# Performance work log

Measured on AMD Instinct MI355X. Metric: run time of the kernel, lower is better.

The kernel has to match this reference:

```python
import jax, jax.numpy as jnp
import numpy as np

B, S, P, D, H, R = 2, 2048, 1024, 2048, 16, 16
DH = D // H  # 128


def _rope(t, cos, sin):
    # t: [B,S,H,DH]; cos/sin: [S, DH//2]; complex pair rotation
    t2 = t.reshape(t.shape[0], t.shape[1], t.shape[2], DH // 2, 2)
    a, b = t2[..., 0], t2[..., 1]
    c = cos[None, :, None, :]
    s = sin[None, :, None, :]
    out = jnp.stack([a * c - b * s, a * s + b * c], axis=-1)
    return out.reshape(t.shape)


def setup_inputs() -> dict:
    key = jax.random.key(0)
    ks = jax.random.split(key, 16)
    sc = 1.0 / np.sqrt(D)
    inv_freq = 1.0 / (10000.0 ** (np.arange(0, DH, 2, dtype=np.float32) / DH))
    pos = (P + np.arange(S, dtype=np.float32))[:, None] * inv_freq[None, :]
    i_idx = np.arange(S)[:, None]
    j_idx = np.arange(P + S)[None, :]
    mask = np.where(j_idx <= P + i_idx, 0.0, -1e9).astype(np.float32)
    return {
        "x": jax.random.normal(ks[0], (B, S, D), jnp.float32),
        "freqs_cos": jnp.asarray(np.cos(pos)),
        "freqs_sin": jnp.asarray(np.sin(pos)),
        "mask": jnp.asarray(mask)[None, None],
        "prev_key": jax.random.normal(ks[1], (B, P, H, DH), jnp.float32),
        "prev_value": jax.random.normal(ks[2], (B, P, H, DH), jnp.float32),
        "pooled_scale": jax.random.uniform(ks[3], (B, 1), jnp.float32),
        "wq": jax.random.normal(ks[4], (D, D), jnp.float32) * sc,
        "wk": jax.random.normal(ks[5], (D, D), jnp.float32) * sc,
        "wv": jax.random.normal(ks[6], (D, D), jnp.float32) * sc,
        "wo": jax.random.normal(ks[7], (D, D), jnp.float32) * sc,
        "wq_A": jax.random.normal(ks[8], (D, R), jnp.float32) * sc,
        "wq_B": jax.random.normal(ks[9], (R, D), jnp.float32) * 0.02,
        "wk_A": jax.random.normal(ks[10], (D, R), jnp.float32) * sc,
        "wk_B": jax.random.normal(ks[11], (R, D), jnp.float32) * 0.02,
        "wv_A": jax.random.normal(ks[12], (D, R), jnp.float32) * sc,
        "wv_B": jax.random.normal(ks[13], (R, D), jnp.float32) * 0.02,
        "wo_A": jax.random.normal(ks[14], (D, R), jnp.float32) * sc,
        "wo_B": jax.random.normal(ks[15], (R, D), jnp.float32) * 0.02,
    }


def reference(x, freqs_cos, freqs_sin, mask, prev_key, prev_value, pooled_scale,
              wq, wk, wv, wo, wq_A, wq_B, wk_A, wk_B, wv_A, wv_B, wo_A, wo_B):
    ps = pooled_scale[:, None, :]  # [B,1,1] per-batch LoRA scale
    xq = x @ wq.T + (x @ wq_A) @ wq_B * ps
    xk = x @ wk.T + (x @ wk_A) @ wk_B * ps
    xv = x @ wv.T + (x @ wv_A) @ wv_B * ps
    xq = xq.reshape(B, S, H, DH)
    xk = xk.reshape(B, S, H, DH)
    xv = xv.reshape(B, S, H, DH)
    xq = _rope(xq, freqs_cos, freqs_sin)
    xk = _rope(xk, freqs_cos, freqs_sin)
    keys = jnp.concatenate([prev_key, xk], axis=1)      # [B,P+S,H,DH]
    values = jnp.concatenate([prev_value, xv], axis=1)
    q = xq.transpose(0, 2, 1, 3)       # [B,H,S,DH]
    k = keys.transpose(0, 2, 1, 3)     # [B,H,P+S,DH]
    v = values.transpose(0, 2, 1, 3)
    scores = jnp.einsum("bhqd,bhkd->bhqk", q, k) / jnp.sqrt(jnp.float32(DH))
    scores = scores + mask
    probs = jax.nn.softmax(scores.astype(jnp.float32), axis=-1).astype(q.dtype)
    out = jnp.einsum("bhqk,bhkd->bhqd", probs, v)
    out = out.transpose(0, 2, 1, 3).reshape(B, S, D)
    return out @ wo.T + (out @ wo_A) @ wo_B * ps
```

## Files before the change

### kernel.cpp

```cpp
#include <hip/hip_runtime.h>
#include <stdint.h>

#define BB 2
#define SS 2048
#define PP 1024
#define DD 2048
#define HH 16
#define RR 16
#define DHH 128
#define TT (PP + SS)
#define BSR (BB * SS)

typedef __attribute__((ext_vector_type(8))) _Float16 half8;
typedef __attribute__((ext_vector_type(4))) float f32x4;

typedef __attribute__((address_space(3))) unsigned int lds_uint;
typedef const __attribute__((address_space(1))) unsigned int glb_uint;
__device__ __forceinline__ void async_copy16(const void* g, void* l) {
    __builtin_amdgcn_global_load_lds((glb_uint*)g, (lds_uint*)l, 16, 0, 0);
}

__global__ __launch_bounds__(256) void cvt_f16_kernel(
    const float* __restrict__ in, _Float16* __restrict__ out, int n4)
{
    int idx = blockIdx.x * 256 + threadIdx.x;
    int stride = gridDim.x * 256;
    for (int c = idx; c < n4; c += stride) {
        float4 v = *(const float4*)(in + (size_t)c * 4);
        union { _Float16 h[4]; uint2 u; } o;
        o.h[0] = (_Float16)v.x; o.h[1] = (_Float16)v.y;
        o.h[2] = (_Float16)v.z; o.h[3] = (_Float16)v.w;
        *(uint2*)(out + (size_t)c * 4) = o.u;
    }
}

__global__ __launch_bounds__(256) void lora_t_kernel(
    const float* __restrict__ A,
    const float* __restrict__ w0, const float* __restrict__ w1,
    const float* __restrict__ w2,
    float* __restrict__ tout)
{
    const float* wA = (blockIdx.z == 0) ? w0 : (blockIdx.z == 1) ? w1 : w2;
    int i  = blockIdx.x * 16 + (threadIdx.x >> 4);
    int r  = threadIdx.x & 15;
    int k0 = blockIdx.y * 512;
    const float* arow = A  + (size_t)i  * DD + k0;
    const float* wcol = wA + (size_t)k0 * RR + r;
    float acc = 0.f;
#pragma unroll 4
    for (int k = 0; k < 512; ++k)
        acc += arow[k] * wcol[k * RR];
    atomicAdd(&tout[(size_t)blockIdx.z * (BSR * RR) + (size_t)i * RR + r], acc);
}

__global__ __launch_bounds__(256) void lora_t_f16_kernel(
    const _Float16* __restrict__ A, const float* __restrict__ wA,
    float* __restrict__ tout)
{
    int i  = blockIdx.x * 16 + (threadIdx.x >> 4);
    int r  = threadIdx.x & 15;
    int k0 = blockIdx.y * 512;
    const _Float16* arow = A + (size_t)i * DD + k0;
    const float* wcol = wA + (size_t)k0 * RR + r;
    float acc = 0.f;
#pragma unroll 4
    for (int k = 0; k < 512; ++k)
        acc += (float)arow[k] * wcol[k * RR];
    atomicAdd(&tout[(size_t)i * RR + r], acc);
}

__global__ __launch_bounds__(256, 3) void gemm_f16_kernel(
    const _Float16* __restrict__ Ah, const _Float16* __restrict__ Wh,
    float* __restrict__ o0, float* __restrict__ o1, float* __restrict__ o2)
{
    __shared__ __align__(16) _Float16 As[128 * 32];
    __shared__ __align__(16) _Float16 Bs[128 * 32];
    const int tid  = threadIdx.x;
    const int wv   = tid >> 6;
    const int lane = tid & 63;
    const int ln   = lane & 15;
    const int quad = lane >> 4;
    const int i0   = blockIdx.x * 128;
    const int j0f  = blockIdx.y * 128;
    const int mat  = j0f >> 11;
    const int jloc = j0f & 2047;
    float* out_f = (mat == 0) ? o0 : (mat == 1) ? o1 : o2;
    const int mb   = (wv >> 1) * 4;
    const int nb   = (wv & 1) * 4;
    const int srow = wv * 32 + (lane >> 2);
    const int scol = (lane & 3) * 8;

    f32x4 zero = {0.f, 0.f, 0.f, 0.f};
    f32x4 acc[4][4];
#pragma unroll
    for (int a = 0; a < 4; ++a)
#pragma unroll
        for (int c = 0; c < 4; ++c) acc[a][c] = zero;

    const _Float16* gA = Ah + (size_t)(i0 + srow) * DD + scol;
    const _Float16* gB = Wh + (size_t)(j0f + srow) * DD + scol;
    _Float16* lA0 = As + (wv * 32) * 32;
    _Float16* lA1 = As + (wv * 32 + 16) * 32;
    _Float16* lB0 = Bs + (wv * 32) * 32;
    _Float16* lB1 = Bs + (wv * 32 + 16) * 32;

    for (int k0 = 0; k0 < DD; k0 += 32) {
        async_copy16(gA + k0, lA0);
        async_copy16(gA + (size_t)16 * DD + k0, lA1);
        async_copy16(gB + k0, lB0);
        async_copy16(gB + (size_t)16 * DD + k0, lB1);
        __syncthreads();
        half8 b[4];
#pragma unroll
        for (int nt = 0; nt < 4; ++nt)
            b[nt] = *(const half8*)&Bs[((nb + nt) * 16 + ln) * 32 + quad * 8];
#pragma unroll
        for (int mt = 0; mt < 4; ++mt) {
            half8 a = *(const half8*)&As[((mb + mt) * 16 + ln) * 32 + quad * 8];
#pragma unroll
            for (int nt = 0; nt < 4; ++nt)
                acc[mt][nt] = __builtin_amdgcn_mfma_f32_16x16x32_f16(a, b[nt], acc[mt][nt], 0, 0, 0);
        }
        __syncthreads();
    }

#pragma unroll
    for (int mt = 0; mt < 4; ++mt)
#pragma unroll
        for (int nt = 0; nt < 4; ++nt)
#pragma unroll
            for (int reg = 0; reg < 4; ++reg) {
                int row = i0 + (mb + mt) * 16 + quad * 4 + reg;
                int col = jloc + (nb + nt) * 16 + ln;
                out_f[(size_t)row * DD + col] = acc[mt][nt][reg];
            }
}

__global__ __launch_bounds__(256) void lora_add_kernel(
    const float* __restrict__ t, const float* __restrict__ wB,
    const float* __restrict__ ps, float* __restrict__ out)
{
    const int n4 = BSR * (DD / 4);
    int idx = blockIdx.x * 256 + threadIdx.x;
    int stride = gridDim.x * 256;
    for (int c = idx; c < n4; c += stride) {
        int i  = c >> 9;
        int j4 = c & 511;
        float psb = ps[i >> 11];
        const float* trow = t + (size_t)i * RR;
        float* op = out + (size_t)i * DD + j4 * 4;
        f32x4 acc = *(const f32x4*)op;
#pragma unroll
        for (int r = 0; r < 16; ++r) {
            float tv = psb * trow[r];
            f32x4 w = *(const f32x4*)(wB + (size_t)r * DD + j4 * 4);
#pragma unroll
            for (int q = 0; q < 4; ++q)
                acc[q] += tv * w[q];
        }
        *(f32x4*)op = acc;
    }
}

__global__ __launch_bounds__(256) void prev_scatter_kernel(
    const float* __restrict__ pk, const float* __restrict__ pv,
    _Float16* __restrict__ kh, _Float16* __restrict__ vTh)
{
    __shared__ __align__(16) _Float16 vt[128][72];
    const int pt = blockIdx.x, h = blockIdx.y;
    const int b = pt >> 4, p0 = (pt & 15) * 64;
    const int tid = threadIdx.x;
    const size_t bh = (size_t)(b * HH + h);
#pragma unroll
    for (int p = 0; p < 8; ++p) {
        int c = tid + 256 * p;
        int pl = c >> 5, c4 = (c & 31) * 4;
        float4 v4 = *(const float4*)(pk + (((size_t)(b * PP + p0 + pl)) * HH + h) * DHH + c4);
        union { _Float16 h4[4]; uint2 u; } o;
        o.h4[0] = (_Float16)v4.x; o.h4[1] = (_Float16)v4.y;
        o.h4[2] = (_Float16)v4.z; o.h4[3] = (_Float16)v4.w;
        *(uint2*)(kh + (bh * TT + p0 + pl) * DHH + c4) = o.u;
    }
#pragma unroll
    for (int p = 0; p < 8; ++p) {
        int c = tid + 256 * p;
        int pl = c >> 5, c4 = (c & 31) * 4;
        float4 v4 = *(const float4*)(pv + (((size_t)(b * PP + p0 + pl)) * HH + h) * DHH + c4);
        vt[c4 + 0][pl] = (_Float16)v4.x;
        vt[c4 + 1][pl] = (_Float16)v4.y;
        vt[c4 + 2][pl] = (_Float16)v4.z;
        vt[c4 + 3][pl] = (_Float16)v4.w;
    }
    __syncthreads();
#pragma unroll
    for (int p = 0; p < 4; ++p) {
        int c = tid + 256 * p;
        int d = c >> 3, c8 = (c & 7) * 8;
        *(half8*)(vTh + (bh * DHH + d) * TT + p0 + c8) = *(const half8*)&vt[d][c8];
    }
}

__global__ __launch_bounds__(256) void rope_scatter_kernel(
    const float* __restrict__ xq, const float* __restrict__ xk,
    const float* __restrict__ xv,
    const float* __restrict__ t_all,
    const float* __restrict__ wqB, const float* __restrict__ wkB,
    const float* __restrict__ wvB,
    const float* __restrict__ ps,
    const float* __restrict__ fcos, const float* __restrict__ fsin,
    _Float16* __restrict__ qh, _Float16* __restrict__ kh,
    _Float16* __restrict__ vTh)
{
    __shared__ float tS[64][48];
    __shared__ float wBs[3][16][128];
    __shared__ __align__(16) _Float16 vt[128][72];
    const int st = blockIdx.x, h = blockIdx.y;
    const int i0 = st * 64;
    const int b  = i0 >> 11;
    const int s0 = i0 & 2047;
    const int tid = threadIdx.x;
    const size_t bh = (size_t)(b * HH + h);
    const float QSC = 0.12753102f;

#pragma unroll
    for (int p = 0; p < 12; ++p) {
        int idx = tid + 256 * p;
        int w = idx >> 10, rem = idx & 1023;
        int sl = rem >> 4, r = rem & 15;
        tS[sl][w * 16 + r] = t_all[(size_t)w * (BSR * RR) + (size_t)(i0 + sl) * RR + r];
    }
#pragma unroll
    for (int w = 0; w < 3; ++w) {
        const float* src = (w == 0) ? wqB : (w == 1) ? wkB : wvB;
#pragma unroll
        for (int p = 0; p < 8; ++p) {
            int idx = tid + 256 * p;
            int r = idx >> 7, dd = idx & 127;
            wBs[w][r][dd] = src[(size_t)r * DD + h * DHH + dd];
        }
    }
    __syncthreads();
    const float psb = ps[b];

#pragma unroll
    for (int w = 0; w < 2; ++w) {
        const float* src = (w == 0) ? xq : xk;
        for (int p = 0; p < 16; ++p) {
            int pp = tid + 256 * p;
            int sl = pp >> 6, dd = pp & 63;
            int d = dd * 2;
            int i = i0 + sl, s = s0 + sl;
            float2 pr = *(const float2*)(src + (size_t)i * DD + h * DHH + d);
            float a = pr.x, b2 = pr.y;
            float la = 0.f, lb = 0.f;
#pragma unroll
            for (int r = 0; r < 16; ++r) {
                float tv = tS[sl][w * 16 + r];
                la += tv * wBs[w][r][d];
                lb += tv * wBs[w][r][d + 1];
            }
            a  += psb * la;
            b2 += psb * lb;
            float c  = fcos[(size_t)s * 64 + dd];
            float sn = fsin[(size_t)s * 64 + dd];
            float na = a * c - b2 * sn;
            float nb = a * sn + b2 * c;
            union { _Float16 h2[2]; unsigned u; } o;
            if (w == 0) {
                o.h2[0] = (_Float16)(na * QSC); o.h2[1] = (_Float16)(nb * QSC);
                *(unsigned*)(qh + (bh * SS + s) * DHH + d) = o.u;
            } else {
                o.h2[0] = (_Float16)na; o.h2[1] = (_Float16)nb;
                *(unsigned*)(kh + (bh * TT + PP + s) * DHH + d) = o.u;
            }
        }
    }
    for (int p = 0; p < 16; ++p) {
        int pp = tid + 256 * p;
        int sl = pp >> 6, dd = pp & 63;
        int d = dd * 2;
        int i = i0 + sl;
        float2 pr = *(const float2*)(xv + (size_t)i * DD + h * DHH + d);
        float a = pr.x, b2 = pr.y;
        float la = 0.f, lb = 0.f;
#pragma unroll
        for (int r = 0; r < 16; ++r) {
            float tv = tS[sl][32 + r];
            la += tv * wBs[2][r][d];
            lb += tv * wBs[2][r][d + 1];
        }
        a  += psb * la;
        b2 += psb * lb;
        vt[d][sl]     = (_Float16)a;
        vt[d + 1][sl] = (_Float16)b2;
    }
    __syncthreads();
#pragma unroll
    for (int p = 0; p < 4; ++p) {
        int c = tid + 256 * p;
        int d = c >> 3, c8 = (c & 7) * 8;
        *(half8*)(vTh + (bh * DHH + d) * TT + PP + s0 + c8) = *(const half8*)&vt[d][c8];
    }
}

__global__ __launch_bounds__(256) void attn_kernel(
    const _Float16* __restrict__ qh, const _Float16* __restrict__ kh,
    const _Float16* __restrict__ vTh, _Float16* __restrict__ attn_h)
{
    __shared__ __align__(16) _Float16 k_lds[64][136];
    __shared__ __align__(16) _Float16 v_lds[128][72];
    __shared__ __align__(16) _Float16 p_lds[4][2][16][72];
    const int lin = blockIdx.x;
    int bh_i, qt;
    if (lin < 256) { bh_i = lin & 31; qt = lin >> 5; }
    else { int l2 = lin - 256; bh_i = l2 & 31; qt = 15 - (l2 >> 5); }
    const int h = bh_i & 15, b = bh_i >> 4;
    const int qbase = qt * 128;
    const int tid = threadIdx.x, wv = tid >> 6, lane = tid & 63;
    const int ln = lane & 15, quad = lane >> 4;
    const size_t bh = (size_t)(b * HH + h);

    half8 qfrag[2][4];
#pragma unroll
    for (int mt = 0; mt < 2; ++mt) {
        const _Float16* qrow = qh + (bh * SS + qbase + wv * 32 + mt * 16 + ln) * DHH;
#pragma unroll
        for (int ks = 0; ks < 4; ++ks)
            qfrag[mt][ks] = *(const half8*)(qrow + ks * 32 + quad * 8);
    }
    f32x4 zero = {0.f, 0.f, 0.f, 0.f};
    f32x4 O[2][8];
#pragma unroll
    for (int mt = 0; mt < 2; ++mt)
#pragma unroll
        for (int i = 0; i < 8; ++i) O[mt][i] = zero;
    float l_part[2][4];
#pragma unroll
    for (int mt = 0; mt < 2; ++mt)
#pragma unroll
        for (int r = 0; r < 4; ++r) l_part[mt][r] = 0.f;

    const int ntiles = 18 + 2 * qt;
    for (int kt = 0; kt < ntiles; ++kt) {
        const int kb = kt * 64;
#pragma unroll
        for (int p = 0; p < 4; ++p) {
            int c = tid + 256 * p;
            int key = c >> 4, c8 = (c & 15) * 8;
            *(half8*)&k_lds[key][c8] = *(const half8*)(kh + (bh * TT + kb + key) * DHH + c8);
        }
#pragma unroll
        for (int p = 0; p < 4; ++p) {
            int c = tid + 256 * p;
            int d = c >> 3, c8 = (c & 7) * 8;
            *(half8*)&v_lds[d][c8] = *(const half8*)(vTh + (bh * DHH + d) * TT + kb + c8);
        }
        __syncthreads();

        f32x4 sv[2][4];
#pragma unroll
        for (int nt = 0; nt < 4; ++nt) {
            half8 kf[4];
#pragma unroll
            for (int ks = 0; ks < 4; ++ks)
                kf[ks] = *(const half8*)&k_lds[nt * 16 + ln][ks * 32 + quad * 8];
#pragma unroll
            for (int mt = 0; mt < 2; ++mt) {
                f32x4 s = zero;
#pragma unroll
                for (int ks = 0; ks < 4; ++ks)
                    s = __builtin_amdgcn_mfma_f32_16x16x32_f16(qfrag[mt][ks], kf[ks], s, 0, 0, 0);
                sv[mt][nt] = s;
            }
        }

        const bool tail = (kt >= ntiles - 2);
#pragma unroll
        for (int mt = 0; mt < 2; ++mt)
#pragma unroll
            for (int nt = 0; nt < 4; ++nt)
#pragma unroll
                for (int reg = 0; reg < 4; ++reg) {
                    float z = sv[mt][nt][reg];
                    if (tail) {
                        int jj = kb + nt * 16 + ln;
                        int rg = PP + qbase + wv * 32 + mt * 16 + quad * 4 + reg;
                        if (jj > rg) z = -1e30f;
                    }
                    float p = exp2f(z - 12.f);
                    l_part[mt][reg] += p;
                    p_lds[wv][mt][quad * 4 + reg][nt * 16 + ln] = (_Float16)p;
                }

#pragma unroll
        for (int kf2 = 0; kf2 < 2; ++kf2) {
            half8 pa0 = *(const half8*)&p_lds[wv][0][ln][kf2 * 32 + quad * 8];
            half8 pa1 = *(const half8*)&p_lds[wv][1][ln][kf2 * 32 + quad * 8];
#pragma unroll
            for (int d8 = 0; d8 < 8; ++d8) {
                half8 vb = *(const half8*)&v_lds[d8 * 16 + ln][kf2 * 32 + quad * 8];
                O[0][d8] = __builtin_amdgcn_mfma_f32_16x16x32_f16(pa0, vb, O[0][d8], 0, 0, 0);
                O[1][d8] = __builtin_amdgcn_mfma_f32_16x16x32_f16(pa1, vb, O[1][d8], 0, 0, 0);
            }
        }
        __syncthreads();
    }

#pragma unroll
    for (int mt = 0; mt < 2; ++mt)
#pragma unroll
        for (int reg = 0; reg < 4; ++reg) {
            float l = l_part[mt][reg];
#pragma unroll
            for (int off = 1; off < 16; off <<= 1)
                l += __shfl_xor(l, off);
            l_part[mt][reg] = 1.f / l;
        }
#pragma unroll
    for (int mt = 0; mt < 2; ++mt)
#pragma unroll
        for (int d8 = 0; d8 < 8; ++d8)
#pragma unroll
            for (int reg = 0; reg < 4; ++reg) {
                int row = qbase + wv * 32 + mt * 16 + quad * 4 + reg;
                int col = h * DHH + d8 * 16 + ln;
                attn_h[((size_t)b * SS + row) * DD + col] =
                    (_Float16)(O[mt][d8][reg] * l_part[mt][reg]);
            }
}

extern "C" void kernel_launch(void* const* d_in, const int* in_sizes, int n_in,
                              void* d_out, int out_size, void* d_ws, size_t ws_size,
                              hipStream_t stream) {
    const float* x    = (const float*)d_in[0];
    const float* fcos = (const float*)d_in[1];
    const float* fsin = (const float*)d_in[2];
    const float* pk   = (const float*)d_in[4];
    const float* pv   = (const float*)d_in[5];
    const float* ps   = (const float*)d_in[6];
    const float* wq   = (const float*)d_in[7];
    const float* wk   = (const float*)d_in[8];
    const float* wvw  = (const float*)d_in[9];
    const float* wo   = (const float*)d_in[10];
    const float* wqA  = (const float*)d_in[11];
    const float* wqB  = (const float*)d_in[12];
    const float* wkA  = (const float*)d_in[13];
    const float* wkB  = (const float*)d_in[14];
    const float* wvA  = (const float*)d_in[15];
    const float* wvB  = (const float*)d_in[16];
    const float* woA  = (const float*)d_in[17];
    const float* woB  = (const float*)d_in[18];
    float* out = (float*)d_out;

    float* t_all = (float*)d_ws;
    float* t_o   = t_all + 3 * BSR * RR;
    float* xq    = t_all + 4 * BSR * RR;
    float* xk    = xq + (size_t)BSR * DD;
    float* xv    = xk + (size_t)BSR * DD;
    _Float16* xh    = (_Float16*)(xv + (size_t)BSR * DD);
    _Float16* wqkvh = xh + (size_t)BSR * DD;
    _Float16* woh   = wqkvh + (size_t)3 * DD * DD;
    _Float16* qh_   = woh + (size_t)DD * DD;
    _Float16* kh_   = qh_ + (size_t)BB * HH * SS * DHH;
    _Float16* vTh   = kh_ + (size_t)BB * HH * TT * DHH;
    _Float16* attn_h = vTh + (size_t)BB * HH * DHH * TT;
    (void)ws_size; (void)in_sizes; (void)n_in; (void)out_size;

    hipMemsetAsync(t_all, 0, (size_t)4 * BSR * RR * sizeof(float), stream);

    cvt_f16_kernel<<<512, 256, 0, stream>>>(x,   xh, (BSR * DD) / 4);
    cvt_f16_kernel<<<512, 256, 0, stream>>>(wq,  wqkvh,                       (DD * DD) / 4);
    cvt_f16_kernel<<<512, 256, 0, stream>>>(wk,  wqkvh + (size_t)DD * DD,     (DD * DD) / 4);
    cvt_f16_kernel<<<512, 256, 0, stream>>>(wvw, wqkvh + (size_t)2 * DD * DD, (DD * DD) / 4);
    cvt_f16_kernel<<<512, 256, 0, stream>>>(wo,  woh, (DD * DD) / 4);

    lora_t_kernel<<<dim3(256, 4, 3), 256, 0, stream>>>(x, wqA, wkA, wvA, t_all);

    gemm_f16_kernel<<<dim3(32, 48), 256, 0, stream>>>(xh, wqkvh, xq, xk, xv);

    prev_scatter_kernel<<<dim3(32, 16), 256, 0, stream>>>(pk, pv, kh_, vTh);

    rope_scatter_kernel<<<dim3(64, 16), 256, 0, stream>>>(xq, xk, xv, t_all,
                                                          wqB, wkB, wvB, ps,
                                                          fcos, fsin,
                                                          qh_, kh_, vTh);

    attn_kernel<<<512, 256, 0, stream>>>(qh_, kh_, vTh, attn_h);

    lora_t_f16_kernel<<<dim3(256, 4), 256, 0, stream>>>(attn_h, woA, t_o);

    gemm_f16_kernel<<<dim3(32, 16), 256, 0, stream>>>(attn_h, woh, out, out, out);

    lora_add_kernel<<<2048, 256, 0, stream>>>(t_o, woB, ps, out);
}
```

Measured before the change: 826.0 us.

## Register-prefetch next K/V tile, swizzle P LDS layout, add MFMA priority hints

```diff
diff --git a/kernel.cpp b/kernel.cpp
--- a/kernel.cpp
+++ b/kernel.cpp
@@ -340,71 +340,108 @@
 #pragma unroll
         for (int r = 0; r < 4; ++r) l_part[mt][r] = 0.f;
 
+    int offKg[4], offKl[4], offVg[4], offVl[4];
+#pragma unroll
+    for (int p = 0; p < 4; ++p) {
+        int c = tid + 256 * p;
+        int key = c >> 4, ck = (c & 15) * 8;
+        offKg[p] = key * DHH + ck;
+        offKl[p] = key * 136 + ck;
+        int d = c >> 3, cv = (c & 7) * 8;
+        offVg[p] = d * TT + cv;
+        offVl[p] = d * 72 + cv;
+    }
+    const _Float16* kbase = kh + bh * (size_t)TT * DHH;
+    const _Float16* vbase = vTh + bh * (size_t)DHH * TT;
+
     const int ntiles = 18 + 2 * qt;
-    for (int kt = 0; kt < ntiles; ++kt) {
-        const int kb = kt * 64;
-#pragma unroll
-        for (int p = 0; p < 4; ++p) {
-            int c = tid + 256 * p;
-            int key = c >> 4, c8 = (c & 15) * 8;
-            *(half8*)&k_lds[key][c8] = *(const half8*)(kh + (bh * TT + kb + key) * DHH + c8);
-        }
-#pragma unroll
-        for (int p = 0; p < 4; ++p) {
-            int c = tid + 256 * p;
-            int d = c >> 3, c8 = (c & 7) * 8;
-            *(half8*)&v_lds[d][c8] = *(const half8*)(vTh + (bh * DHH + d) * TT + kb + c8);
-        }
-        __syncthreads();
-
-        f32x4 sv[2][4];
-#pragma unroll
-        for (int nt = 0; nt < 4; ++nt) {
-            half8 kf[4];
-#pragma unroll
-            for (int ks = 0; ks < 4; ++ks)
-                kf[ks] = *(const half8*)&k_lds[nt * 16 + ln][ks * 32 + quad * 8];
-#pragma unroll
-            for (int mt = 0; mt < 2; ++mt) {
-                f32x4 s = zero;
-#pragma unroll
-                for (int ks = 0; ks < 4; ++ks)
-                    s = __builtin_amdgcn_mfma_f32_16x16x32_f16(qfrag[mt][ks], kf[ks], s, 0, 0, 0);
-                sv[mt][nt] = s;
-            }
-        }
-
-        const bool tail = (kt >= ntiles - 2);
-#pragma unroll
-        for (int mt = 0; mt < 2; ++mt)
-#pragma unroll
-            for (int nt = 0; nt < 4; ++nt)
-#pragma unroll
-                for (int reg = 0; reg < 4; ++reg) {
-                    float z = sv[mt][nt][reg];
-                    if (tail) {
-                        int jj = kb + nt * 16 + ln;
-                        int rg = PP + qbase + wv * 32 + mt * 16 + quad * 4 + reg;
-                        if (jj > rg) z = -1e30f;
-                    }
-                    float p = exp2f(z - 12.f);
-                    l_part[mt][reg] += p;
-                    p_lds[wv][mt][quad * 4 + reg][nt * 16 + ln] = (_Float16)p;
-                }
-
-#pragma unroll
-        for (int kf2 = 0; kf2 < 2; ++kf2) {
-            half8 pa0 = *(const half8*)&p_lds[wv][0][ln][kf2 * 32 + quad * 8];
-            half8 pa1 = *(const half8*)&p_lds[wv][1][ln][kf2 * 32 + quad * 8];
-#pragma unroll
-            for (int d8 = 0; d8 < 8; ++d8) {
-                half8 vb = *(const half8*)&v_lds[d8 * 16 + ln][kf2 * 32 + quad * 8];
-                O[0][d8] = __builtin_amdgcn_mfma_f32_16x16x32_f16(pa0, vb, O[0][d8], 0, 0, 0);
-                O[1][d8] = __builtin_amdgcn_mfma_f32_16x16x32_f16(pa1, vb, O[1][d8], 0, 0, 0);
-            }
-        }
-        __syncthreads();
-    }
+
+    half8 k0r[4], v0r[4], k1r[4], v1r[4];
+#pragma unroll
+    for (int p = 0; p < 4; ++p) {
+        k0r[p] = *(const half8*)(kbase + offKg[p]);
+        v0r[p] = *(const half8*)(vbase + offVg[p]);
+    }
+
+#define ATTN_BODY(KT, KC, VC, KN, VN)                                          \
+  {                                                                            \
+    const int kb = (KT) * 64;                                                  \
+    _Pragma("unroll")                                                          \
+    for (int p = 0; p < 4; ++p) {                                              \
+        *(half8*)((_Float16*)k_lds + offKl[p]) = KC[p];                        \
+        *(half8*)((_Float16*)v_lds + offVl[p]) = VC[p];                        \
+    }                                                                          \
+    __syncthreads();                                                           \
+    if ((KT) + 1 < ntiles) {                                                   \
+        const _Float16* kg = kbase + (size_t)(kb + 64) * DHH;                  \
+        const _Float16* vg = vbase + (kb + 64);                                \
+        _Pragma("unroll")                                                      \
+        for (int p = 0; p < 4; ++p) {                                          \
+            KN[p] = *(const half8*)(kg + offKg[p]);                            \
+            VN[p] = *(const half8*)(vg + offVg[p]);                            \
+        }                                                                      \
+    }                                                                          \
+    f32x4 sv[2][4];                                                            \
+    __builtin_amdgcn_s_setprio(1);                                             \
+    _Pragma("unroll")                                                          \
+    for (int nt = 0; nt < 4; ++nt) {                                           \
+        half8 kf[4];                                                           \
+        _Pragma("unroll")                                                      \
+        for (int ks = 0; ks < 4; ++ks)                                         \
+            kf[ks] = *(const half8*)&k_lds[nt * 16 + ln][ks * 32 + quad * 8];  \
+        _Pragma("unroll")                                                      \
+        for (int mt = 0; mt < 2; ++mt) {                                       \
+            f32x4 s = zero;                                                    \
+            _Pragma("unroll")                                                  \
+            for (int ks = 0; ks < 4; ++ks)                                     \
+                s = __builtin_amdgcn_mfma_f32_16x16x32_f16(qfrag[mt][ks], kf[ks], s, 0, 0, 0); \
+            sv[mt][nt] = s;                                                    \
+        }                                                                      \
+    }                                                                          \
+    __builtin_amdgcn_s_setprio(0);                                             \
+    const bool tail = ((KT) >= ntiles - 2);                                    \
+    _Pragma("unroll")                                                          \
+    for (int mt = 0; mt < 2; ++mt)                                             \
+        _Pragma("unroll")                                                      \
+        for (int nt = 0; nt < 4; ++nt)                                         \
+            _Pragma("unroll")                                                  \
+            for (int reg = 0; reg < 4; ++reg) {                                \
+                float z = sv[mt][nt][reg];                                     \
+                if (tail) {                                                    \
+                    int jj = kb + nt * 16 + ln;                                \
+                    int rg = PP + qbase + wv * 32 + mt * 16 + quad * 4 + reg;  \
+                    if (jj > rg) z = -1e30f;                                   \
+                }                                                              \
+                float pz = exp2f(z - 12.f);                                    \
+                l_part[mt][reg] += pz;                                         \
+                {                                                              \
+                    int row = quad * 4 + reg;                                  \
+                    int cs  = (nt * 2 + (ln >> 3)) ^ ((row >> 1) & 7);         \
+                    p_lds[wv][mt][row][cs * 8 + (ln & 7)] = (_Float16)pz;      \
+                }                                                              \
+            }                                                                  \
+    __builtin_amdgcn_s_setprio(1);                                             \
+    _Pragma("unroll")                                                          \
+    for (int kf2 = 0; kf2 < 2; ++kf2) {                                        \
+        int cA = ((kf2 * 4 + quad) ^ ((ln >> 1) & 7)) * 8;                     \
+        half8 pa0 = *(const half8*)&p_lds[wv][0][ln][cA];                      \
+        half8 pa1 = *(const half8*)&p_lds[wv][1][ln][cA];                      \
+        _Pragma("unroll")                                                      \
+        for (int d8 = 0; d8 < 8; ++d8) {                                       \
+            half8 vb = *(const half8*)&v_lds[d8 * 16 + ln][kf2 * 32 + quad * 8]; \
+            O[0][d8] = __builtin_amdgcn_mfma_f32_16x16x32_f16(pa0, vb, O[0][d8], 0, 0, 0); \
+            O[1][d8] = __builtin_amdgcn_mfma_f32_16x16x32_f16(pa1, vb, O[1][d8], 0, 0, 0); \
+        }                                                                      \
+    }                                                                          \
+    __builtin_amdgcn_s_setprio(0);                                             \
+    __syncthreads();                                                           \
+  }
+
+    for (int kt = 0; kt < ntiles; kt += 2) {
+        ATTN_BODY(kt,     k0r, v0r, k1r, v1r);
+        ATTN_BODY(kt + 1, k1r, v1r, k0r, v0r);
+    }
+#undef ATTN_BODY
 
 #pragma unroll
     for (int mt = 0; mt < 2; ++mt)
```

New measurement: 766.0 us. -7.3%, faster.
